# Kernel tuning notes

Measured on AMD Instinct MI355X. Metric: run time of the kernel, lower is better.

## Reference

```python
import jax, jax.numpy as jnp
import numpy as np

NEG_SLOPE = 0.1

def leaky(z):
    return jnp.where(z >= 0, z, NEG_SLOPE * z)

def setup_inputs() -> dict:
    key = jax.random.key(0)
    ks = jax.random.split(key, 7)
    N, F = 8192, 256
    s = 1.0 / np.sqrt(F)
    return {
        "x": jax.random.normal(ks[0], (N, F), dtype=jnp.float32),
        "W3": jax.random.normal(ks[1], (1, 2 * F), dtype=jnp.float32) * (1.0 / np.sqrt(2 * F)),
        "b3": jax.random.normal(ks[2], (1,), dtype=jnp.float32) * 0.01,
        "W6": jax.random.normal(ks[3], (F, F), dtype=jnp.float32) * s,
        "b6": jax.random.normal(ks[4], (F,), dtype=jnp.float32) * 0.01,
        "W5": jax.random.normal(ks[5], (F, F), dtype=jnp.float32) * s,
        "b5": jax.random.normal(ks[6], (F,), dtype=jnp.float32) * 0.01,
    }

def reference(x, W3, b3, W6, b6, W5, b5):
    # x: [N, F] node features (original: list of N [1,F] tensors)
    N, F = x.shape
    # g3(concat(n_i, n_j)) == x_i @ Wa + x_j @ Wb + b3, so never build [N,N,2F]
    Wa = W3[0, :F]  # [F]
    Wb = W3[0, F:]  # [F]
    s = x @ Wa      # [N] contribution of n_i
    t = x @ Wb      # [N] contribution of n_j
    W = leaky(s[:, None] + t[None, :] + b3[0])  # [N,N] pairwise weights
    G = leaky(x @ W6.T + b6)                    # [N,F] g6(n_j)
    # sum over j != i of W_ij * G_j, averaged by (N-1)
    diag = leaky(s + t + b3[0])                 # [N] W_ii
    M = (W @ G - diag[:, None] * G) / (N - 1)   # [N,F] aggregated message
    out = leaky(M @ W5.T + b5) + x              # g5(message) + residual
    return out
```

## Files before the change

kernel.cpp:

```cpp
#include <hip/hip_runtime.h>
#include <stdint.h>

#define NR 8192
#define FD 256

typedef __attribute__((ext_vector_type(8))) short bf16x8;
typedef __attribute__((ext_vector_type(4))) float f32x4;

__device__ __forceinline__ float leaky_f(float z){ return z >= 0.0f ? z : 0.1f * z; }

__device__ __forceinline__ unsigned short f2bf(float f){
    union { float f; uint32_t u; } v; v.f = f;
    uint32_t r = v.u + 0x7fffu + ((v.u >> 16) & 1u);
    return (unsigned short)(r >> 16);
}
__device__ __forceinline__ float bf2f(unsigned short h){
    union { uint32_t u; float f; } v; v.u = ((uint32_t)h) << 16;
    return v.f;
}

__global__ void k0_prep(const float* __restrict__ W, short* __restrict__ hi,
                        short* __restrict__ lo, int n){
    int i = blockIdx.x * 256 + threadIdx.x;
    if (i < n){
        float v = W[i];
        unsigned short h = f2bf(v);
        hi[i] = (short)h;
        lo[i] = (short)f2bf(v - bf2f(h));
    }
}

__global__ __launch_bounds__(256) void k1_st(const float* __restrict__ x,
                                             const float* __restrict__ W3,
                                             float* __restrict__ s,
                                             float* __restrict__ t,
                                             int* __restrict__ rank){
    int wave = threadIdx.x >> 6;
    int lane = threadIdx.x & 63;
    int row  = blockIdx.x * 4 + wave;
    const float* xr = x + (size_t)row * FD;
    float as = 0.0f, at = 0.0f;
    #pragma unroll
    for (int m = 0; m < 4; ++m){
        int kk = lane + 64 * m;
        float xv = xr[kk];
        as += xv * W3[kk];
        at += xv * W3[FD + kk];
    }
    #pragma unroll
    for (int off = 32; off > 0; off >>= 1){
        as += __shfl_xor(as, off, 64);
        at += __shfl_xor(at, off, 64);
    }
    if (lane == 0){ s[row] = as; t[row] = at; rank[row] = 0; }
}

__global__ __launch_bounds__(256) void k3a_count(const float* __restrict__ t,
                                                 int* __restrict__ rank){
    __shared__ __align__(16) float seg[256];
    int tid = threadIdx.x;
    int j = blockIdx.x * 256 + tid;
    int segBase = blockIdx.y * 256;
    seg[tid] = t[segBase + tid];
    __syncthreads();
    float tj = t[j];
    int cnt = 0;
    #pragma unroll 16
    for (int r = 0; r < 256; r += 4){
        float4 v = *reinterpret_cast<const float4*>(&seg[r]);
        int jp = segBase + r;
        cnt += (v.x < tj) || (v.x == tj && (jp + 0) < j);
        cnt += (v.y < tj) || (v.y == tj && (jp + 1) < j);
        cnt += (v.z < tj) || (v.z == tj && (jp + 2) < j);
        cnt += (v.w < tj) || (v.w == tj && (jp + 3) < j);
    }
    atomicAdd(&rank[j], cnt);
}

__global__ __launch_bounds__(256) void k3b_scatter(const float* __restrict__ t,
                                                   const int* __restrict__ rank,
                                                   float* __restrict__ ts){
    int j = blockIdx.x * 256 + threadIdx.x;
    ts[rank[j]] = t[j];
}

template<bool SCATTER, bool ADD>
__global__ __launch_bounds__(256) void gemm_nt(
    const float* __restrict__ A,
    const short* __restrict__ Whi, const short* __restrict__ Wlo,
    const float* __restrict__ bias,
    const float* __restrict__ addend,
    const int* __restrict__ perm,
    float* __restrict__ out)
{
    int wave = threadIdx.x >> 6;
    int lane = threadIdx.x & 63;
    int rowBase = blockIdx.x * 64 + wave * 16;
    int colBase = blockIdx.y * 128;
    int m16 = lane & 15;
    int k8  = (lane >> 4) * 8;

    f32x4 acc[8];
    #pragma unroll
    for (int c = 0; c < 8; ++c) acc[c] = (f32x4){0.f, 0.f, 0.f, 0.f};

    const float* arow = A + (size_t)(rowBase + m16) * FD + k8;

    #pragma unroll
    for (int ks = 0; ks < 8; ++ks){
        int kb = ks * 32;
        float4 a0 = *reinterpret_cast<const float4*>(arow + kb);
        float4 a1 = *reinterpret_cast<const float4*>(arow + kb + 4);
        float a8[8] = {a0.x, a0.y, a0.z, a0.w, a1.x, a1.y, a1.z, a1.w};
        bf16x8 ahi, alo;
        #pragma unroll
        for (int e = 0; e < 8; ++e){
            unsigned short h = f2bf(a8[e]);
            ahi[e] = (short)h;
            alo[e] = (short)f2bf(a8[e] - bf2f(h));
        }
        #pragma unroll
        for (int c = 0; c < 8; ++c){
            size_t boff = (size_t)(colBase + c * 16 + m16) * FD + k8 + kb;
            bf16x8 bhi = *reinterpret_cast<const bf16x8*>(Whi + boff);
            bf16x8 blo = *reinterpret_cast<const bf16x8*>(Wlo + boff);
            acc[c] = __builtin_amdgcn_mfma_f32_16x16x32_bf16(ahi, bhi, acc[c], 0, 0, 0);
            acc[c] = __builtin_amdgcn_mfma_f32_16x16x32_bf16(alo, bhi, acc[c], 0, 0, 0);
            acc[c] = __builtin_amdgcn_mfma_f32_16x16x32_bf16(ahi, blo, acc[c], 0, 0, 0);
        }
    }

    int rq = (lane >> 4) * 4;
    #pragma unroll
    for (int c = 0; c < 8; ++c){
        int gcol = colBase + c * 16 + m16;
        float bs = bias[gcol];
        #pragma unroll
        for (int j = 0; j < 4; ++j){
            int grow = rowBase + rq + j;
            float v = leaky_f(acc[c][j] + bs);
            if (ADD) v += addend[(size_t)grow * FD + gcol];
            int orow = SCATTER ? perm[grow] : grow;
            out[(size_t)orow * FD + gcol] = v;
        }
    }
}

__global__ __launch_bounds__(256) void k4a_partial(const float* __restrict__ Gs,
                                                   const float* __restrict__ ts,
                                                   float* __restrict__ p0,
                                                   float* __restrict__ p1){
    int col = threadIdx.x;
    int chunk = blockIdx.x;
    int base = chunk * 32;
    float s0 = 0.f, s1 = 0.f;
    #pragma unroll
    for (int r = 0; r < 32; ++r){
        float g = Gs[(size_t)(base + r) * FD + col];
        s0 += g;
        s1 += ts[base + r] * g;
    }
    p0[chunk * FD + col] = s0;
    p1[chunk * FD + col] = s1;
}

__global__ __launch_bounds__(64) void k4b_scan(float* __restrict__ p0,
                                               float* __restrict__ p1,
                                               float* __restrict__ Pex0,
                                               float* __restrict__ Pex1){
    int bid  = blockIdx.x;
    int lane = threadIdx.x;
    float* p  = (bid < 256) ? p0 : p1;
    float* Pt = (bid < 256) ? Pex0 : Pex1;
    int col = bid & 255;
    int c0 = lane * 4;
    float v0 = p[(size_t)(c0 + 0) * FD + col];
    float v1 = p[(size_t)(c0 + 1) * FD + col];
    float v2 = p[(size_t)(c0 + 2) * FD + col];
    float v3 = p[(size_t)(c0 + 3) * FD + col];
    float s1 = v0 + v1, s2 = s1 + v2, s3 = s2 + v3;
    float x = s3;
    #pragma unroll
    for (int off = 1; off < 64; off <<= 1){
        float n = __shfl_up(x, off, 64);
        if (lane >= off) x += n;
    }
    float excl = x - s3;
    p[(size_t)(c0 + 0) * FD + col] = excl;
    p[(size_t)(c0 + 1) * FD + col] = excl + v0;
    p[(size_t)(c0 + 2) * FD + col] = excl + s1;
    p[(size_t)(c0 + 3) * FD + col] = excl + s2;
    if (lane == 63) Pt[(size_t)NR * FD + col] = x;
}

__global__ __launch_bounds__(256) void k4c_fill(const float* __restrict__ Gs,
                                                const float* __restrict__ ts,
                                                const float* __restrict__ p0,
                                                const float* __restrict__ p1,
                                                float* __restrict__ Pex0,
                                                float* __restrict__ Pex1){
    int col = threadIdx.x;
    int chunk = blockIdx.x;
    int base = chunk * 32;
    float run0 = p0[chunk * FD + col];
    float run1 = p1[chunk * FD + col];
    #pragma unroll
    for (int r = 0; r < 32; ++r){
        size_t row = base + r;
        Pex0[row * FD + col] = run0;
        Pex1[row * FD + col] = run1;
        float g = Gs[row * FD + col];
        run0 += g;
        run1 += ts[row] * g;
    }
}

__global__ __launch_bounds__(256) void k5_build_m(
    const float* __restrict__ s, const float* __restrict__ t,
    const float* __restrict__ ts, const int* __restrict__ rank,
    const float* __restrict__ Gs,
    const float* __restrict__ Pex0, const float* __restrict__ Pex1,
    const float* __restrict__ b3, float* __restrict__ M)
{
    __shared__ float lts[NR];
    for (int i = threadIdx.x; i < NR; i += 256) lts[i] = ts[i];
    __syncthreads();
    int col = threadIdx.x;
    float c = b3[0];
    float T0 = Pex0[(size_t)NR * FD + col];
    float T1 = Pex1[(size_t)NR * FD + col];
    const float inv = 1.0f / (float)(NR - 1);
    int rowBase = blockIdx.x * 32;
    for (int r = 0; r < 32; ++r){
        int i = rowBase + r;
        float si = s[i], ti = t[i];
        float sic = si + c;
        float theta = -sic;
        int lo = 0, hi = NR;
        while (lo < hi){
            int mid = (lo + hi) >> 1;
            if (lts[mid] < theta) lo = mid + 1; else hi = mid;
        }
        int pos = lo;
        float P0 = Pex0[(size_t)pos * FD + col];
        float P1 = Pex1[(size_t)pos * FD + col];
        float g  = Gs[(size_t)rank[i] * FD + col];
        float diag = leaky_f(sic + ti);
        float full = sic * T0 + T1;
        float act  = sic * (T0 - P0) + (T1 - P1);
        M[(size_t)i * FD + col] = (0.1f * full + 0.9f * act - diag * g) * inv;
    }
}

extern "C" void kernel_launch(void* const* d_in, const int* in_sizes, int n_in,
                              void* d_out, int out_size, void* d_ws, size_t ws_size,
                              hipStream_t stream)
{
    const float* x  = (const float*)d_in[0];
    const float* W3 = (const float*)d_in[1];
    const float* b3 = (const float*)d_in[2];
    const float* W6 = (const float*)d_in[3];
    const float* b6 = (const float*)d_in[4];
    const float* W5 = (const float*)d_in[5];
    const float* b5 = (const float*)d_in[6];
    float* out = (float*)d_out;

    char* ws = (char*)d_ws;
    size_t off = 0;
    auto alloc = [&](size_t bytes) -> void* {
        void* p = ws + off;
        off += (bytes + 255) & ~(size_t)255;
        return p;
    };
    float* s    = (float*)alloc(NR * 4);
    float* t    = (float*)alloc(NR * 4);
    float* ts   = (float*)alloc(NR * 4);
    int*   rank = (int*)  alloc(NR * 4);
    float* p0   = (float*)alloc(256 * FD * 4);
    float* p1   = (float*)alloc(256 * FD * 4);
    short* W6hi = (short*)alloc(FD * FD * 2);
    short* W6lo = (short*)alloc(FD * FD * 2);
    short* W5hi = (short*)alloc(FD * FD * 2);
    short* W5lo = (short*)alloc(FD * FD * 2);
    float* Gs   = (float*)alloc((size_t)NR * FD * 4);
    float* Pex0 = (float*)alloc((size_t)(NR + 1) * FD * 4);
    float* Pex1 = (float*)alloc((size_t)(NR + 1) * FD * 4);
    float* M    = (float*)alloc((size_t)NR * FD * 4);
    (void)ws_size; (void)in_sizes; (void)n_in; (void)out_size;

    k0_prep<<<dim3(FD * FD / 256), dim3(256), 0, stream>>>(W6, W6hi, W6lo, FD * FD);
    k0_prep<<<dim3(FD * FD / 256), dim3(256), 0, stream>>>(W5, W5hi, W5lo, FD * FD);
    k1_st<<<dim3(NR / 4), dim3(256), 0, stream>>>(x, W3, s, t, rank);
    k3a_count<<<dim3(32, 32), dim3(256), 0, stream>>>(t, rank);
    k3b_scatter<<<dim3(NR / 256), dim3(256), 0, stream>>>(t, rank, ts);
    gemm_nt<true, false><<<dim3(128, 2), dim3(256), 0, stream>>>(
        x, W6hi, W6lo, b6, nullptr, rank, Gs);
    k4a_partial<<<dim3(256), dim3(256), 0, stream>>>(Gs, ts, p0, p1);
    k4b_scan<<<dim3(512), dim3(64), 0, stream>>>(p0, p1, Pex0, Pex1);
    k4c_fill<<<dim3(256), dim3(256), 0, stream>>>(Gs, ts, p0, p1, Pex0, Pex1);
    k5_build_m<<<dim3(NR / 32), dim3(256), 0, stream>>>(
        s, t, ts, rank, Gs, Pex0, Pex1, b3, M);
    gemm_nt<false, true><<<dim3(128, 2), dim3(256), 0, stream>>>(
        M, W5hi, W5lo, b5, x, nullptr, out);
}
```

Baseline: 191.3 us.

## Drop full prefix arrays, recompute partial prefix from chunk sums in build kernel

Removes the materialized per-row prefix arrays Pex0/Pex1 (two 8 MB buffers) and the fill kernel. Instead it keeps chunk-level prefix sums over 8-row chunks and adds up to 7 Gs rows inside the build kernel. The binary search moves into a separate per-row kernel that packs sic, diag, pos and rank into a float4. GEMM tiles shrink to 64 columns so the grid has more blocks, and the s/t dot-product kernel now uses float4 loads. The cost is some extra Gs reads in the build step and a smaller per-block tile in the GEMMs.

```diff
diff --git a/kernel.cpp b/kernel.cpp
--- a/kernel.cpp
+++ b/kernel.cpp
@@ -3,6 +3,7 @@
 
 #define NR 8192
 #define FD 256
+#define NCH 1024
 
 typedef __attribute__((ext_vector_type(8))) short bf16x8;
 typedef __attribute__((ext_vector_type(4))) float f32x4;
@@ -38,15 +39,12 @@
     int wave = threadIdx.x >> 6;
     int lane = threadIdx.x & 63;
     int row  = blockIdx.x * 4 + wave;
-    const float* xr = x + (size_t)row * FD;
-    float as = 0.0f, at = 0.0f;
-    #pragma unroll
-    for (int m = 0; m < 4; ++m){
-        int kk = lane + 64 * m;
-        float xv = xr[kk];
-        as += xv * W3[kk];
-        at += xv * W3[FD + kk];
-    }
+    const float4* xr = (const float4*)(x + (size_t)row * FD);
+    const float4* wa = (const float4*)W3;
+    const float4* wb = (const float4*)(W3 + FD);
+    float4 xv = xr[lane], av = wa[lane], bv = wb[lane];
+    float as = xv.x*av.x + xv.y*av.y + xv.z*av.z + xv.w*av.w;
+    float at = xv.x*bv.x + xv.y*bv.y + xv.z*bv.z + xv.w*bv.w;
     #pragma unroll
     for (int off = 32; off > 0; off >>= 1){
         as += __shfl_xor(as, off, 64);
@@ -95,14 +93,14 @@
 {
     int wave = threadIdx.x >> 6;
     int lane = threadIdx.x & 63;
-    int rowBase = blockIdx.x * 64 + wave * 16;
-    int colBase = blockIdx.y * 128;
+    int rowBase = blockIdx.y * 64 + wave * 16;
+    int colBase = blockIdx.x * 64;
     int m16 = lane & 15;
     int k8  = (lane >> 4) * 8;
 
-    f32x4 acc[8];
-    #pragma unroll
-    for (int c = 0; c < 8; ++c) acc[c] = (f32x4){0.f, 0.f, 0.f, 0.f};
+    f32x4 acc[4];
+    #pragma unroll
+    for (int c = 0; c < 4; ++c) acc[c] = (f32x4){0.f, 0.f, 0.f, 0.f};
 
     const float* arow = A + (size_t)(rowBase + m16) * FD + k8;
 
@@ -120,7 +118,7 @@
             alo[e] = (short)f2bf(a8[e] - bf2f(h));
         }
         #pragma unroll
-        for (int c = 0; c < 8; ++c){
+        for (int c = 0; c < 4; ++c){
             size_t boff = (size_t)(colBase + c * 16 + m16) * FD + k8 + kb;
             bf16x8 bhi = *reinterpret_cast<const bf16x8*>(Whi + boff);
             bf16x8 blo = *reinterpret_cast<const bf16x8*>(Wlo + boff);
@@ -132,7 +130,7 @@
 
     int rq = (lane >> 4) * 4;
     #pragma unroll
-    for (int c = 0; c < 8; ++c){
+    for (int c = 0; c < 4; ++c){
         int gcol = colBase + c * 16 + m16;
         float bs = bias[gcol];
         #pragma unroll
@@ -152,100 +150,92 @@
                                                    float* __restrict__ p1){
     int col = threadIdx.x;
     int chunk = blockIdx.x;
-    int base = chunk * 32;
+    int base = chunk * 8;
     float s0 = 0.f, s1 = 0.f;
     #pragma unroll
-    for (int r = 0; r < 32; ++r){
+    for (int r = 0; r < 8; ++r){
         float g = Gs[(size_t)(base + r) * FD + col];
         s0 += g;
         s1 += ts[base + r] * g;
     }
-    p0[chunk * FD + col] = s0;
-    p1[chunk * FD + col] = s1;
+    p0[(size_t)chunk * FD + col] = s0;
+    p1[(size_t)chunk * FD + col] = s1;
 }
 
 __global__ __launch_bounds__(64) void k4b_scan(float* __restrict__ p0,
-                                               float* __restrict__ p1,
-                                               float* __restrict__ Pex0,
-                                               float* __restrict__ Pex1){
+                                               float* __restrict__ p1){
     int bid  = blockIdx.x;
     int lane = threadIdx.x;
-    float* p  = (bid < 256) ? p0 : p1;
-    float* Pt = (bid < 256) ? Pex0 : Pex1;
+    float* p = (bid < 256) ? p0 : p1;
     int col = bid & 255;
-    int c0 = lane * 4;
-    float v0 = p[(size_t)(c0 + 0) * FD + col];
-    float v1 = p[(size_t)(c0 + 1) * FD + col];
-    float v2 = p[(size_t)(c0 + 2) * FD + col];
-    float v3 = p[(size_t)(c0 + 3) * FD + col];
-    float s1 = v0 + v1, s2 = s1 + v2, s3 = s2 + v3;
-    float x = s3;
+    int c0 = lane * 16;
+    float v[16];
+    #pragma unroll
+    for (int k = 0; k < 16; ++k) v[k] = p[(size_t)(c0 + k) * FD + col];
+    float run = 0.f;
+    #pragma unroll
+    for (int k = 0; k < 16; ++k) run += v[k];
+    float x = run;
     #pragma unroll
     for (int off = 1; off < 64; off <<= 1){
         float n = __shfl_up(x, off, 64);
         if (lane >= off) x += n;
     }
-    float excl = x - s3;
-    p[(size_t)(c0 + 0) * FD + col] = excl;
-    p[(size_t)(c0 + 1) * FD + col] = excl + v0;
-    p[(size_t)(c0 + 2) * FD + col] = excl + s1;
-    p[(size_t)(c0 + 3) * FD + col] = excl + s2;
-    if (lane == 63) Pt[(size_t)NR * FD + col] = x;
-}
-
-__global__ __launch_bounds__(256) void k4c_fill(const float* __restrict__ Gs,
-                                                const float* __restrict__ ts,
-                                                const float* __restrict__ p0,
-                                                const float* __restrict__ p1,
-                                                float* __restrict__ Pex0,
-                                                float* __restrict__ Pex1){
+    float e = x - run;
+    #pragma unroll
+    for (int k = 0; k < 16; ++k){
+        p[(size_t)(c0 + k) * FD + col] = e;
+        e += v[k];
+    }
+    if (lane == 63) p[(size_t)NCH * FD + col] = x;
+}
+
+__global__ __launch_bounds__(256) void k5a_pos(const float* __restrict__ s,
+                                               const float* __restrict__ t,
+                                               const float* __restrict__ b3,
+                                               const float* __restrict__ ts,
+                                               const int* __restrict__ rank,
+                                               float4* __restrict__ scal){
+    int i = blockIdx.x * 256 + threadIdx.x;
+    float c = b3[0];
+    float sic = s[i] + c;
+    float theta = -sic;
+    int lo = 0, hi = NR;
+    while (lo < hi){
+        int mid = (lo + hi) >> 1;
+        if (ts[mid] < theta) lo = mid + 1; else hi = mid;
+    }
+    float diag = leaky_f(sic + t[i]);
+    scal[i] = make_float4(sic, diag, __int_as_float(lo), __int_as_float(rank[i]));
+}
+
+__global__ __launch_bounds__(256) void k5b_build(
+    const float4* __restrict__ scal, const float* __restrict__ ts,
+    const float* __restrict__ Gs,
+    const float* __restrict__ p0, const float* __restrict__ p1,
+    float* __restrict__ M)
+{
     int col = threadIdx.x;
-    int chunk = blockIdx.x;
-    int base = chunk * 32;
-    float run0 = p0[chunk * FD + col];
-    float run1 = p1[chunk * FD + col];
-    #pragma unroll
-    for (int r = 0; r < 32; ++r){
-        size_t row = base + r;
-        Pex0[row * FD + col] = run0;
-        Pex1[row * FD + col] = run1;
-        float g = Gs[row * FD + col];
-        run0 += g;
-        run1 += ts[row] * g;
-    }
-}
-
-__global__ __launch_bounds__(256) void k5_build_m(
-    const float* __restrict__ s, const float* __restrict__ t,
-    const float* __restrict__ ts, const int* __restrict__ rank,
-    const float* __restrict__ Gs,
-    const float* __restrict__ Pex0, const float* __restrict__ Pex1,
-    const float* __restrict__ b3, float* __restrict__ M)
-{
-    __shared__ float lts[NR];
-    for (int i = threadIdx.x; i < NR; i += 256) lts[i] = ts[i];
-    __syncthreads();
-    int col = threadIdx.x;
-    float c = b3[0];
-    float T0 = Pex0[(size_t)NR * FD + col];
-    float T1 = Pex1[(size_t)NR * FD + col];
+    int i0 = blockIdx.x * 8;
+    float T0 = p0[(size_t)NCH * FD + col];
+    float T1 = p1[(size_t)NCH * FD + col];
     const float inv = 1.0f / (float)(NR - 1);
-    int rowBase = blockIdx.x * 32;
-    for (int r = 0; r < 32; ++r){
-        int i = rowBase + r;
-        float si = s[i], ti = t[i];
-        float sic = si + c;
-        float theta = -sic;
-        int lo = 0, hi = NR;
-        while (lo < hi){
-            int mid = (lo + hi) >> 1;
-            if (lts[mid] < theta) lo = mid + 1; else hi = mid;
-        }
-        int pos = lo;
-        float P0 = Pex0[(size_t)pos * FD + col];
-        float P1 = Pex1[(size_t)pos * FD + col];
-        float g  = Gs[(size_t)rank[i] * FD + col];
-        float diag = leaky_f(sic + ti);
+    #pragma unroll
+    for (int r = 0; r < 8; ++r){
+        int i = i0 + r;
+        float4 sc = scal[i];
+        float sic = sc.x, diag = sc.y;
+        int pos = __float_as_int(sc.z);
+        int rk  = __float_as_int(sc.w);
+        int ch  = pos >> 3;
+        float P0 = p0[(size_t)ch * FD + col];
+        float P1 = p1[(size_t)ch * FD + col];
+        for (int r2 = ch * 8; r2 < pos; ++r2){
+            float g2 = Gs[(size_t)r2 * FD + col];
+            P0 += g2;
+            P1 += ts[r2] * g2;
+        }
+        float g = Gs[(size_t)rk * FD + col];
         float full = sic * T0 + T1;
         float act  = sic * (T0 - P0) + (T1 - P1);
         M[(size_t)i * FD + col] = (0.1f * full + 0.9f * act - diag * g) * inv;
@@ -272,20 +262,19 @@
         off += (bytes + 255) & ~(size_t)255;
         return p;
     };
-    float* s    = (float*)alloc(NR * 4);
-    float* t    = (float*)alloc(NR * 4);
-    float* ts   = (float*)alloc(NR * 4);
-    int*   rank = (int*)  alloc(NR * 4);
-    float* p0   = (float*)alloc(256 * FD * 4);
-    float* p1   = (float*)alloc(256 * FD * 4);
-    short* W6hi = (short*)alloc(FD * FD * 2);
-    short* W6lo = (short*)alloc(FD * FD * 2);
-    short* W5hi = (short*)alloc(FD * FD * 2);
-    short* W5lo = (short*)alloc(FD * FD * 2);
-    float* Gs   = (float*)alloc((size_t)NR * FD * 4);
-    float* Pex0 = (float*)alloc((size_t)(NR + 1) * FD * 4);
-    float* Pex1 = (float*)alloc((size_t)(NR + 1) * FD * 4);
-    float* M    = (float*)alloc((size_t)NR * FD * 4);
+    float*  s    = (float*)alloc(NR * 4);
+    float*  t    = (float*)alloc(NR * 4);
+    float*  ts   = (float*)alloc(NR * 4);
+    int*    rank = (int*)  alloc(NR * 4);
+    float*  p0   = (float*)alloc((size_t)(NCH + 1) * FD * 4);
+    float*  p1   = (float*)alloc((size_t)(NCH + 1) * FD * 4);
+    short*  W6hi = (short*)alloc(FD * FD * 2);
+    short*  W6lo = (short*)alloc(FD * FD * 2);
+    short*  W5hi = (short*)alloc(FD * FD * 2);
+    short*  W5lo = (short*)alloc(FD * FD * 2);
+    float4* scal = (float4*)alloc(NR * 16);
+    float*  Gs   = (float*)alloc((size_t)NR * FD * 4);
+    float*  M    = (float*)alloc((size_t)NR * FD * 4);
     (void)ws_size; (void)in_sizes; (void)n_in; (void)out_size;
 
     k0_prep<<<dim3(FD * FD / 256), dim3(256), 0, stream>>>(W6, W6hi, W6lo, FD * FD);
@@ -293,13 +282,12 @@
     k1_st<<<dim3(NR / 4), dim3(256), 0, stream>>>(x, W3, s, t, rank);
     k3a_count<<<dim3(32, 32), dim3(256), 0, stream>>>(t, rank);
     k3b_scatter<<<dim3(NR / 256), dim3(256), 0, stream>>>(t, rank, ts);
-    gemm_nt<true, false><<<dim3(128, 2), dim3(256), 0, stream>>>(
+    gemm_nt<true, false><<<dim3(FD / 64, NR / 64), dim3(256), 0, stream>>>(
         x, W6hi, W6lo, b6, nullptr, rank, Gs);
-    k4a_partial<<<dim3(256), dim3(256), 0, stream>>>(Gs, ts, p0, p1);
-    k4b_scan<<<dim3(512), dim3(64), 0, stream>>>(p0, p1, Pex0, Pex1);
-    k4c_fill<<<dim3(256), dim3(256), 0, stream>>>(Gs, ts, p0, p1, Pex0, Pex1);
-    k5_build_m<<<dim3(NR / 32), dim3(256), 0, stream>>>(
-        s, t, ts, rank, Gs, Pex0, Pex1, b3, M);
-    gemm_nt<false, true><<<dim3(128, 2), dim3(256), 0, stream>>>(
+    k4a_partial<<<dim3(NCH), dim3(256), 0, stream>>>(Gs, ts, p0, p1);
+    k4b_scan<<<dim3(512), dim3(64), 0, stream>>>(p0, p1);
+    k5a_pos<<<dim3(NR / 256), dim3(256), 0, stream>>>(s, t, b3, ts, rank, scal);
+    k5b_build<<<dim3(NR / 8), dim3(256), 0, stream>>>(scal, ts, Gs, p0, p1, M);
+    gemm_nt<false, true><<<dim3(FD / 64, NR / 64), dim3(256), 0, stream>>>(
         M, W5hi, W5lo, b5, x, nullptr, out);
 }
```

After: 172.2 us. -10.0%, faster.
